# Kernel optimization log

Measured on AMD Instinct MI355X. Metric: run time of the kernel, lower is better.

Reference implementation:

```python
import jax, jax.numpy as jnp
import numpy as np

B, L, DIM, DFF = 4, 2048, 1024, 4096
EPS = 1e-5

def setup_inputs() -> dict:
    key = jax.random.key(0)
    ks = jax.random.split(key, 10)
    s = 0.02
    return {
        "x": jax.random.normal(ks[0], (B, L, DIM), dtype=jnp.float32),
        "ln_g": jnp.ones((DIM,), jnp.float32),
        "ln_b": jnp.zeros((DIM,), jnp.float32),
        "phazor": jax.random.normal(ks[1], (DIM, 2), dtype=jnp.float32),
        "phazor_init": jax.random.normal(ks[2], (DIM, 2), dtype=jnp.float32),
        "w1": jax.random.normal(ks[3], (DIM, DFF), dtype=jnp.float32) * s,
        "b1": jnp.zeros((DFF,), jnp.float32),
        "w2": jax.random.normal(ks[4], (DFF, DIM), dtype=jnp.float32) * s,
        "b2": jnp.zeros((DIM,), jnp.float32),
        "last_conv_re": jax.random.normal(ks[5], (B, DIM), dtype=jnp.float32),
        "last_conv_im": jax.random.normal(ks[6], (B, DIM), dtype=jnp.float32),
    }

def layer_norm(x, g, b):
    mu = jnp.mean(x, axis=-1, keepdims=True)
    var = jnp.var(x, axis=-1, keepdims=True)
    return (x - mu) * jax.lax.rsqrt(var + EPS) * g + b

def spiral_conv(x, phazor, phazor_init, last_re, last_im):
    # x: [B, L, D] float32
    Lx = x.shape[1]
    p = jax.lax.complex(phazor[:, 0], phazor[:, 1])          # [D]
    p_init = jax.lax.complex(phazor_init[:, 0], phazor_init[:, 1])
    pa = jnp.abs(p)
    p = p / pa * jnp.exp(-pa)                                 # normalized decay phazor
    t = jnp.arange(Lx)
    prog = p[None, :] ** t[:, None]                           # [L, D] p^t
    filt = prog * p_init[None, :]                             # [L, D]
    ffilt = jnp.fft.fft(filt, n=2 * Lx, axis=0)               # [2L, D]
    xf = jnp.fft.fft(x.astype(jnp.complex64), n=2 * Lx, axis=1)  # [B, 2L, D]
    conv = jnp.fft.ifft(ffilt[None] * xf, axis=1)[:, :Lx]     # [B, L, D]
    last = jax.lax.complex(last_re, last_im)                  # [B, D] (detached state)
    conv_with_past = conv + last[:, None, :] * prog[None] * p[None, None, :]
    return conv_with_past.real

def reference(x, ln_g, ln_b, phazor, phazor_init, w1, b1, w2, b2, last_conv_re, last_conv_im):
    x_ = x
    h = layer_norm(x, ln_g, ln_b)
    h = spiral_conv(h, phazor, phazor_init, last_conv_re, last_conv_im)
    x = h + x_
    x_ = x
    h = layer_norm(x, ln_g, ln_b)  # same LayerNorm params reused, as in the source
    h = jax.nn.silu(h @ w1 + b1) @ w2 + b2  # FFN, dropout=0 (eval)
    return h + x_

if __name__ == "__main__":
    out = reference(**setup_inputs())
    print(out.shape, out.dtype)
```

## Files before the change

### kernel.cpp

```cpp
#include <hip/hip_runtime.h>
#include <stdint.h>
#include <stddef.h>

#define DIMC 1024
#define LSEQ 2048
#define BSZ  4
#define DFFC 4096
#define NTOK (BSZ*LSEQ)
#define NCHUNK 32
#define CHUNK 64

typedef __bf16 bf16x8 __attribute__((ext_vector_type(8)));
typedef float  f32x4  __attribute__((ext_vector_type(4)));

__device__ __forceinline__ unsigned short f2bf(float f) {
  unsigned int u = __float_as_uint(f);
  u += 0x7fffu + ((u >> 16) & 1u);
  return (unsigned short)(u >> 16);
}

__device__ __forceinline__ void async16(const void* g, void* l) {
  __builtin_amdgcn_global_load_lds(
      (const __attribute__((address_space(1))) unsigned int*)(uintptr_t)g,
      (__attribute__((address_space(3))) unsigned int*)(uintptr_t)l,
      16, 0, 0);
}

__global__ __launch_bounds__(256) void ln_stats(const float* __restrict__ x,
                                                float* __restrict__ mu,
                                                float* __restrict__ rstd) {
  const int token = blockIdx.x;
  const float4* xp = (const float4*)(x + (size_t)token * DIMC);
  float4 v = xp[threadIdx.x];
  float s  = v.x + v.y + v.z + v.w;
  float s2 = v.x*v.x + v.y*v.y + v.z*v.z + v.w*v.w;
  #pragma unroll
  for (int o = 32; o; o >>= 1) { s += __shfl_down(s, o); s2 += __shfl_down(s2, o); }
  __shared__ float sh[8];
  const int lane = threadIdx.x & 63, w = threadIdx.x >> 6;
  if (lane == 0) { sh[w] = s; sh[4 + w] = s2; }
  __syncthreads();
  if (threadIdx.x == 0) {
    float ts  = sh[0] + sh[1] + sh[2] + sh[3];
    float ts2 = sh[4] + sh[5] + sh[6] + sh[7];
    float m = ts * (1.f / DIMC);
    float var = ts2 * (1.f / DIMC) - m * m;
    mu[token] = m;
    rstd[token] = rsqrtf(var + 1e-5f);
  }
}

__global__ __launch_bounds__(256) void ln_apply_bf16(const float* __restrict__ x,
                                                     const float* __restrict__ mu,
                                                     const float* __restrict__ rstd,
                                                     const float* __restrict__ g,
                                                     const float* __restrict__ bb,
                                                     unsigned short* __restrict__ out) {
  const size_t i = (size_t)blockIdx.x * 256 + threadIdx.x;
  float4 v = ((const float4*)x)[i];
  const int token = (int)(i >> 8);
  const int d4 = (int)(i & 255);
  float4 gv = ((const float4*)g)[d4];
  float4 bv = ((const float4*)bb)[d4];
  const float m = mu[token], r = rstd[token];
  ushort4 o;
  o.x = f2bf((v.x - m) * r * gv.x + bv.x);
  o.y = f2bf((v.y - m) * r * gv.y + bv.y);
  o.z = f2bf((v.z - m) * r * gv.z + bv.z);
  o.w = f2bf((v.w - m) * r * gv.w + bv.w);
  ((ushort4*)out)[i] = o;
}

__global__ __launch_bounds__(256) void transpose_bf16(const float* __restrict__ w,
                                                      unsigned short* __restrict__ wt,
                                                      int K, int N) {
  __shared__ float tile[32][33];
  const int n0 = blockIdx.x * 32, k0 = blockIdx.y * 32;
  const int tx = threadIdx.x, ty = threadIdx.y;
  #pragma unroll
  for (int i = 0; i < 32; i += 8)
    tile[ty + i][tx] = w[(size_t)(k0 + ty + i) * N + n0 + tx];
  __syncthreads();
  #pragma unroll
  for (int i = 0; i < 32; i += 8)
    wt[(size_t)(n0 + ty + i) * K + k0 + tx] = f2bf(tile[tx][ty + i]);
}

__device__ __forceinline__ void get_p(const float* __restrict__ phazor, int d,
                                      float& p_re, float& p_im) {
  float pre = phazor[2 * d], pim = phazor[2 * d + 1];
  float a = sqrtf(pre * pre + pim * pim);
  float sc = expf(-a) / a;
  p_re = pre * sc;
  p_im = pim * sc;
}

__global__ __launch_bounds__(256) void scan_phase1(const float* __restrict__ x,
                                                   const float* __restrict__ mu,
                                                   const float* __restrict__ rstd,
                                                   const float* __restrict__ g,
                                                   const float* __restrict__ bb,
                                                   const float* __restrict__ phazor,
                                                   float* __restrict__ Sre,
                                                   float* __restrict__ Sim) {
  const int d = blockIdx.x * 256 + threadIdx.x;
  const int c = blockIdx.y;
  const int b = blockIdx.z;
  float p_re, p_im; get_p(phazor, d, p_re, p_im);
  const float gd = g[d], bd = bb[d];
  const int t0 = c * CHUNK;
  const float* xp  = x + ((size_t)(b * LSEQ + t0)) * DIMC + d;
  const float* mup = mu + b * LSEQ + t0;
  const float* rp  = rstd + b * LSEQ + t0;
  float r_re = 0.f, r_im = 0.f;
  #pragma unroll 4
  for (int s = 0; s < CHUNK; ++s) {
    float hv = (xp[(size_t)s * DIMC] - mup[s]) * rp[s] * gd + bd;
    float nr = p_re * r_re - p_im * r_im + hv;
    float ni = p_re * r_im + p_im * r_re;
    r_re = nr; r_im = ni;
  }
  const int bd_i = b * DIMC + d;
  Sre[c * (BSZ * DIMC) + bd_i] = r_re;
  Sim[c * (BSZ * DIMC) + bd_i] = r_im;
}

__global__ __launch_bounds__(256) void scan_phase2(const float* __restrict__ phazor,
                                                   const float* __restrict__ Sre,
                                                   const float* __restrict__ Sim,
                                                   float* __restrict__ Cre,
                                                   float* __restrict__ Cim) {
  const int bd = blockIdx.x * 256 + threadIdx.x;
  const int d = bd & (DIMC - 1);
  float p_re, p_im; get_p(phazor, d, p_re, p_im);
  float br = p_re, bi = p_im;
  #pragma unroll
  for (int i = 0; i < 6; ++i) { float t = br * br - bi * bi; bi = 2.f * br * bi; br = t; }
  float R_re = 0.f, R_im = 0.f;
  for (int c = 0; c < NCHUNK; ++c) {
    Cre[c * (BSZ * DIMC) + bd] = R_re;
    Cim[c * (BSZ * DIMC) + bd] = R_im;
    float sre = Sre[c * (BSZ * DIMC) + bd], sim = Sim[c * (BSZ * DIMC) + bd];
    float nr = br * R_re - bi * R_im + sre;
    float ni = br * R_im + bi * R_re + sim;
    R_re = nr; R_im = ni;
  }
}

__global__ __launch_bounds__(256) void scan_phase3(const float* __restrict__ x,
                                                   const float* __restrict__ mu,
                                                   const float* __restrict__ rstd,
                                                   const float* __restrict__ g,
                                                   const float* __restrict__ bb,
                                                   const float* __restrict__ phazor,
                                                   const float* __restrict__ phazor_init,
                                                   const float* __restrict__ last_re,
                                                   const float* __restrict__ last_im,
                                                   const float* __restrict__ Cre,
                                                   const float* __restrict__ Cim,
                                                   float* __restrict__ x2) {
  const int d = blockIdx.x * 256 + threadIdx.x;
  const int c = blockIdx.y;
  const int b = blockIdx.z;
  float p_re, p_im; get_p(phazor, d, p_re, p_im);
  const float pi_re = phazor_init[2 * d], pi_im = phazor_init[2 * d + 1];
  const float gd = g[d], bd_ = bb[d];
  const int bd_i = b * DIMC + d;
  float r_re = Cre[c * (BSZ * DIMC) + bd_i];
  float r_im = Cim[c * (BSZ * DIMC) + bd_i];
  float br = p_re, bi = p_im;
  #pragma unroll
  for (int i = 0; i < 6; ++i) { float t = br * br - bi * bi; bi = 2.f * br * bi; br = t; }
  float er = 1.f, ei = 0.f;
  int e = c;
  while (e) {
    if (e & 1) { float t = er * br - ei * bi; ei = er * bi + ei * br; er = t; }
    float t2 = br * br - bi * bi; bi = 2.f * br * bi; br = t2;
    e >>= 1;
  }
  const float lre = last_re[bd_i], lim = last_im[bd_i];
  float q_re = lre * er - lim * ei;
  float q_im = lre * ei + lim * er;
  const int t0 = c * CHUNK;
  const float* xp  = x + ((size_t)(b * LSEQ + t0)) * DIMC + d;
  const float* mup = mu + b * LSEQ + t0;
  const float* rp  = rstd + b * LSEQ + t0;
  float* op = x2 + ((size_t)(b * LSEQ + t0)) * DIMC + d;
  #pragma unroll 4
  for (int s = 0; s < CHUNK; ++s) {
    float xv = xp[(size_t)s * DIMC];
    float hv = (xv - mup[s]) * rp[s] * gd + bd_;
    float nr = p_re * r_re - p_im * r_im + hv;
    float ni = p_re * r_im + p_im * r_re;
    r_re = nr; r_im = ni;
    float nq = p_re * q_re - p_im * q_im;
    q_im = p_re * q_im + p_im * q_re;
    q_re = nq;
    op[(size_t)s * DIMC] = pi_re * r_re - pi_im * r_im + q_re + xv;
  }
}

template <int EPI>
__global__ __launch_bounds__(256) void gemm_bt(const unsigned short* __restrict__ A,
                                               const unsigned short* __restrict__ Bt,
                                               const float* __restrict__ bias,
                                               const float* __restrict__ resid,
                                               void* __restrict__ outp,
                                               int M, int N, int K) {
  __shared__ __align__(16) unsigned short As[128 * 64];
  __shared__ __align__(16) unsigned short Bs[128 * 64];
  const int tid = threadIdx.x;
  const int lane = tid & 63;
  const int bid = blockIdx.x;
  const int ntn = N >> 7;
  const int tm = (bid / ntn) << 7;
  const int tn = (bid % ntn) << 7;
  const int wave = tid >> 6;
  const int wm = (wave & 1) << 6;
  const int wn = (wave >> 1) << 6;

  f32x4 acc[4][4];
  #pragma unroll
  for (int i = 0; i < 4; ++i)
    #pragma unroll
    for (int j = 0; j < 4; ++j) acc[i][j] = (f32x4){0.f, 0.f, 0.f, 0.f};

  const int o0 = tid * 16;
  for (int k0 = 0; k0 < K; k0 += 64) {
    #pragma unroll
    for (int c = 0; c < 4; ++c) {
      const int o = o0 + c * 4096;
      const int r = o >> 7;
      const int ce = (o & 127) >> 1;
      async16(A  + (size_t)(tm + r) * K + (k0 + ce), (char*)As + o);
      async16(Bt + (size_t)(tn + r) * K + (k0 + ce), (char*)Bs + o);
    }
    __syncthreads();
    #pragma unroll
    for (int kk = 0; kk < 2; ++kk) {
      bf16x8 av[4], bv[4];
      #pragma unroll
      for (int i = 0; i < 4; ++i)
        av[i] = *reinterpret_cast<const bf16x8*>(
            As + ((wm + i * 16 + (lane & 15)) << 6) + kk * 32 + ((lane >> 4) << 3));
      #pragma unroll
      for (int i = 0; i < 4; ++i)
        bv[i] = *reinterpret_cast<const bf16x8*>(
            Bs + ((wn + i * 16 + (lane & 15)) << 6) + kk * 32 + ((lane >> 4) << 3));
      #pragma unroll
      for (int mi = 0; mi < 4; ++mi)
        #pragma unroll
        for (int ni = 0; ni < 4; ++ni)
          acc[mi][ni] = __builtin_amdgcn_mfma_f32_16x16x32_bf16(av[mi], bv[ni], acc[mi][ni], 0, 0, 0);
    }
    __syncthreads();
  }

  const int rgrp = (lane >> 4) << 2;
  #pragma unroll
  for (int ni = 0; ni < 4; ++ni) {
    const int n = tn + wn + ni * 16 + (lane & 15);
    const float bv = bias[n];
    #pragma unroll
    for (int mi = 0; mi < 4; ++mi) {
      const int rb = tm + wm + mi * 16 + rgrp;
      #pragma unroll
      for (int j = 0; j < 4; ++j) {
        float v = acc[mi][ni][j] + bv;
        if constexpr (EPI == 0) {
          v = v / (1.f + __expf(-v));
          ((unsigned short*)outp)[(size_t)(rb + j) * N + n] = f2bf(v);
        } else {
          v += resid[(size_t)(rb + j) * N + n];
          ((float*)outp)[(size_t)(rb + j) * N + n] = v;
        }
      }
    }
  }
}

extern "C" void kernel_launch(void* const* d_in, const int* in_sizes, int n_in,
                              void* d_out, int out_size, void* d_ws, size_t ws_size,
                              hipStream_t stream) {
  const float* x           = (const float*)d_in[0];
  const float* ln_g        = (const float*)d_in[1];
  const float* ln_b        = (const float*)d_in[2];
  const float* phazor      = (const float*)d_in[3];
  const float* phazor_init = (const float*)d_in[4];
  const float* w1          = (const float*)d_in[5];
  const float* b1          = (const float*)d_in[6];
  const float* w2          = (const float*)d_in[7];
  const float* b2          = (const float*)d_in[8];
  const float* last_re     = (const float*)d_in[9];
  const float* last_im     = (const float*)d_in[10];
  float* out = (float*)d_out;
  char* ws = (char*)d_ws;
  const size_t MB = 1ull << 20;

  float* x2  = (float*)(ws);
  float* mu1 = (float*)(ws + 32 * MB);
  float* rs1 = (float*)(ws + 32 * MB + 64 * 1024);
  float* mu2 = (float*)(ws + 32 * MB + 128 * 1024);
  float* rs2 = (float*)(ws + 32 * MB + 192 * 1024);
  float* Sre = (float*)(ws + 32 * MB + 256 * 1024);
  float* Sim = (float*)(ws + 32 * MB + 768 * 1024);
  float* Cre = (float*)(ws + 32 * MB + 1280 * 1024);
  float* Cim = (float*)(ws + 32 * MB + 1792 * 1024);
  unsigned short* h2  = (unsigned short*)(ws + 35 * MB);
  unsigned short* hid = (unsigned short*)(ws + 51 * MB);
  unsigned short* w1t = (unsigned short*)(ws + 115 * MB);
  unsigned short* w2t = (unsigned short*)(ws + 123 * MB);

  transpose_bf16<<<dim3(DFFC / 32, DIMC / 32), dim3(32, 8), 0, stream>>>(w1, w1t, DIMC, DFFC);
  transpose_bf16<<<dim3(DIMC / 32, DFFC / 32), dim3(32, 8), 0, stream>>>(w2, w2t, DFFC, DIMC);

  ln_stats<<<NTOK, 256, 0, stream>>>(x, mu1, rs1);
  scan_phase1<<<dim3(DIMC / 256, NCHUNK, BSZ), 256, 0, stream>>>(x, mu1, rs1, ln_g, ln_b, phazor, Sre, Sim);
  scan_phase2<<<(BSZ * DIMC) / 256, 256, 0, stream>>>(phazor, Sre, Sim, Cre, Cim);
  scan_phase3<<<dim3(DIMC / 256, NCHUNK, BSZ), 256, 0, stream>>>(x, mu1, rs1, ln_g, ln_b, phazor,
                                                                 phazor_init, last_re, last_im,
                                                                 Cre, Cim, x2);
  ln_stats<<<NTOK, 256, 0, stream>>>(x2, mu2, rs2);
  ln_apply_bf16<<<NTOK, 256, 0, stream>>>(x2, mu2, rs2, ln_g, ln_b, h2);

  gemm_bt<0><<<(NTOK / 128) * (DFFC / 128), 256, 0, stream>>>(h2, w1t, b1, nullptr, hid, NTOK, DFFC, DIMC);
  gemm_bt<1><<<(NTOK / 128) * (DIMC / 128), 256, 0, stream>>>(hid, w2t, b2, x2, out, NTOK, DIMC, DFFC);
}
```

Measured before the change: 378.9 us.

## Replace FFN GEMMs with 8-wave double-buffered pipelined 256-row tile kernel

```diff
diff --git a/kernel.cpp b/kernel.cpp
--- a/kernel.cpp
+++ b/kernel.cpp
@@ -25,6 +25,16 @@
       (__attribute__((address_space(3))) unsigned int*)(uintptr_t)l,
       16, 0, 0);
 }
+
+__device__ __forceinline__ void bar() {
+  asm volatile("" ::: "memory");
+  __builtin_amdgcn_s_barrier();
+  asm volatile("" ::: "memory");
+}
+#define LGKM0 do { asm volatile("s_waitcnt lgkmcnt(0)" ::: "memory"); \
+                   __builtin_amdgcn_sched_barrier(0); } while (0)
+#define VMCNT(n) asm volatile("s_waitcnt vmcnt(" #n ")" ::: "memory")
+#define MFMA_BF16 __builtin_amdgcn_mfma_f32_16x16x32_bf16
 
 __global__ __launch_bounds__(256) void ln_stats(const float* __restrict__ x,
                                                 float* __restrict__ mu,
@@ -200,70 +210,232 @@
   }
 }
 
-template <int EPI>
-__global__ __launch_bounds__(256) void gemm_bt(const unsigned short* __restrict__ A,
-                                               const unsigned short* __restrict__ Bt,
-                                               const float* __restrict__ bias,
-                                               const float* __restrict__ resid,
-                                               void* __restrict__ outp,
-                                               int M, int N, int K) {
-  __shared__ __align__(16) unsigned short As[128 * 64];
-  __shared__ __align__(16) unsigned short Bs[128 * 64];
-  const int tid = threadIdx.x;
+template<int BN, int EPI>
+__global__ __launch_bounds__(512, 2) void gemm8(const unsigned short* __restrict__ A,
+                                                const unsigned short* __restrict__ Bt,
+                                                const float* __restrict__ bias,
+                                                const float* __restrict__ resid,
+                                                void* __restrict__ outp,
+                                                int M, int N, int K) {
+  constexpr int AUS = 256 * 32;
+  constexpr int BUS = BN * 32;
+  constexpr int BUFUS = 2 * AUS + 2 * BUS;
+  constexpr int NI = BN / 64;
+  __shared__ __align__(16) unsigned short lds[2 * BUFUS];
+
+  const int tid  = threadIdx.x;
   const int lane = tid & 63;
-  const int bid = blockIdx.x;
-  const int ntn = N >> 7;
-  const int tm = (bid / ntn) << 7;
-  const int tn = (bid % ntn) << 7;
   const int wave = tid >> 6;
-  const int wm = (wave & 1) << 6;
-  const int wn = (wave >> 1) << 6;
-
-  f32x4 acc[4][4];
-  #pragma unroll
-  for (int i = 0; i < 4; ++i)
+  const int wm = (wave & 1) * 128;
+  const int wn = (wave >> 1) * (BN / 4);
+  const int r15 = lane & 15;
+  const int cus = ((lane >> 4) ^ ((r15 >> 1) & 3)) * 8;
+
+  int bid = blockIdx.x;
+  const int cpx = gridDim.x >> 3;
+  bid = (bid & 7) * cpx + (bid >> 3);
+  const int ntn = N / BN;
+  const int tm = (bid / ntn) * 256;
+  const int tn = (bid % ntn) * BN;
+  const int NT = K >> 6;
+
+  f32x4 acc[8][NI];
+  #pragma unroll
+  for (int i = 0; i < 8; ++i)
     #pragma unroll
-    for (int j = 0; j < 4; ++j) acc[i][j] = (f32x4){0.f, 0.f, 0.f, 0.f};
-
-  const int o0 = tid * 16;
-  for (int k0 = 0; k0 < K; k0 += 64) {
+    for (int j = 0; j < NI; ++j) acc[i][j] = (f32x4){0.f, 0.f, 0.f, 0.f};
+
+  auto stageA = [&](int buf, int kk, int k0) {
+    unsigned short* blk = lds + buf * BUFUS + kk * AUS;
+    const unsigned short* g = A + (size_t)tm * K + k0 + kk * 32;
     #pragma unroll
-    for (int c = 0; c < 4; ++c) {
-      const int o = o0 + c * 4096;
-      const int r = o >> 7;
-      const int ce = (o & 127) >> 1;
-      async16(A  + (size_t)(tm + r) * K + (k0 + ce), (char*)As + o);
-      async16(Bt + (size_t)(tn + r) * K + (k0 + ce), (char*)Bs + o);
+    for (int r = 0; r < 2; ++r) {
+      const int s = r * 512 + tid;
+      const int row = s >> 2;
+      const int cg = (s & 3) ^ ((s >> 3) & 3);
+      async16(g + (size_t)row * K + cg * 8, blk + (size_t)s * 8);
     }
-    __syncthreads();
+  };
+  auto stageB = [&](int buf, int kk, int k0) {
+    unsigned short* blk = lds + buf * BUFUS + 2 * AUS + kk * BUS;
+    const unsigned short* g = Bt + (size_t)tn * K + k0 + kk * 32;
     #pragma unroll
-    for (int kk = 0; kk < 2; ++kk) {
-      bf16x8 av[4], bv[4];
-      #pragma unroll
-      for (int i = 0; i < 4; ++i)
-        av[i] = *reinterpret_cast<const bf16x8*>(
-            As + ((wm + i * 16 + (lane & 15)) << 6) + kk * 32 + ((lane >> 4) << 3));
-      #pragma unroll
-      for (int i = 0; i < 4; ++i)
-        bv[i] = *reinterpret_cast<const bf16x8*>(
-            Bs + ((wn + i * 16 + (lane & 15)) << 6) + kk * 32 + ((lane >> 4) << 3));
-      #pragma unroll
-      for (int mi = 0; mi < 4; ++mi)
-        #pragma unroll
-        for (int ni = 0; ni < 4; ++ni)
-          acc[mi][ni] = __builtin_amdgcn_mfma_f32_16x16x32_bf16(av[mi], bv[ni], acc[mi][ni], 0, 0, 0);
+    for (int r = 0; r < BN / 128; ++r) {
+      const int s = r * 512 + tid;
+      const int row = s >> 2;
+      const int cg = (s & 3) ^ ((s >> 3) & 3);
+      async16(g + (size_t)row * K + cg * 8, blk + (size_t)s * 8);
     }
-    __syncthreads();
-  }
-
-  const int rgrp = (lane >> 4) << 2;
-  #pragma unroll
-  for (int ni = 0; ni < 4; ++ni) {
-    const int n = tn + wn + ni * 16 + (lane & 15);
+  };
+  auto rdA = [&](int buf, int kk, int mi) -> bf16x8 {
+    return *(const bf16x8*)(lds + buf * BUFUS + kk * AUS + (wm + mi * 16 + r15) * 32 + cus);
+  };
+  auto rdB = [&](int buf, int kk, int ni) -> bf16x8 {
+    return *(const bf16x8*)(lds + buf * BUFUS + 2 * AUS + kk * BUS + (wn + ni * 16 + r15) * 32 + cus);
+  };
+
+  bf16x8 af[8], bq0, bq1;
+
+  stageA(0, 0, 0); stageB(0, 0, 0); stageA(0, 1, 0); stageB(0, 1, 0);
+  if constexpr (BN == 256) VMCNT(4); else VMCNT(3);
+  bar();
+
+  for (int t = 0; t < NT - 1; ++t) {
+    const int buf = t & 1, nb = buf ^ 1, kn = (t + 1) << 6;
+    if constexpr (BN == 256) {
+      #pragma unroll
+      for (int mi = 0; mi < 8; ++mi) af[mi] = rdA(buf, 0, mi);
+      bq0 = rdB(buf, 0, 0); bq1 = rdB(buf, 0, 1);
+      stageA(nb, 0, kn);
+      bar(); LGKM0;
+      __builtin_amdgcn_s_setprio(1);
+      #pragma unroll
+      for (int mi = 0; mi < 8; ++mi) {
+        acc[mi][0] = MFMA_BF16(af[mi], bq0, acc[mi][0], 0, 0, 0);
+        acc[mi][1] = MFMA_BF16(af[mi], bq1, acc[mi][1], 0, 0, 0);
+      }
+      __builtin_amdgcn_s_setprio(0);
+      bar();
+      bq0 = rdB(buf, 0, 2); bq1 = rdB(buf, 0, 3);
+      stageB(nb, 0, kn);
+      bar(); LGKM0;
+      __builtin_amdgcn_s_setprio(1);
+      #pragma unroll
+      for (int mi = 0; mi < 8; ++mi) {
+        acc[mi][2] = MFMA_BF16(af[mi], bq0, acc[mi][2], 0, 0, 0);
+        acc[mi][3] = MFMA_BF16(af[mi], bq1, acc[mi][3], 0, 0, 0);
+      }
+      __builtin_amdgcn_s_setprio(0);
+      VMCNT(4);
+      bar();
+      #pragma unroll
+      for (int mi = 0; mi < 8; ++mi) af[mi] = rdA(buf, 1, mi);
+      bq0 = rdB(buf, 1, 0); bq1 = rdB(buf, 1, 1);
+      stageA(nb, 1, kn);
+      bar(); LGKM0;
+      __builtin_amdgcn_s_setprio(1);
+      #pragma unroll
+      for (int mi = 0; mi < 8; ++mi) {
+        acc[mi][0] = MFMA_BF16(af[mi], bq0, acc[mi][0], 0, 0, 0);
+        acc[mi][1] = MFMA_BF16(af[mi], bq1, acc[mi][1], 0, 0, 0);
+      }
+      __builtin_amdgcn_s_setprio(0);
+      bar();
+      bq0 = rdB(buf, 1, 2); bq1 = rdB(buf, 1, 3);
+      stageB(nb, 1, kn);
+      bar(); LGKM0;
+      __builtin_amdgcn_s_setprio(1);
+      #pragma unroll
+      for (int mi = 0; mi < 8; ++mi) {
+        acc[mi][2] = MFMA_BF16(af[mi], bq0, acc[mi][2], 0, 0, 0);
+        acc[mi][3] = MFMA_BF16(af[mi], bq1, acc[mi][3], 0, 0, 0);
+      }
+      __builtin_amdgcn_s_setprio(0);
+      VMCNT(4);
+      bar();
+    } else {
+      #pragma unroll
+      for (int mi = 0; mi < 8; ++mi) af[mi] = rdA(buf, 0, mi);
+      bq0 = rdB(buf, 0, 0); bq1 = rdB(buf, 0, 1);
+      stageA(nb, 0, kn); stageB(nb, 0, kn);
+      bar(); LGKM0;
+      __builtin_amdgcn_s_setprio(1);
+      #pragma unroll
+      for (int mi = 0; mi < 8; ++mi) {
+        acc[mi][0] = MFMA_BF16(af[mi], bq0, acc[mi][0], 0, 0, 0);
+        acc[mi][1] = MFMA_BF16(af[mi], bq1, acc[mi][1], 0, 0, 0);
+      }
+      __builtin_amdgcn_s_setprio(0);
+      VMCNT(3);
+      bar();
+      #pragma unroll
+      for (int mi = 0; mi < 8; ++mi) af[mi] = rdA(buf, 1, mi);
+      bq0 = rdB(buf, 1, 0); bq1 = rdB(buf, 1, 1);
+      stageA(nb, 1, kn); stageB(nb, 1, kn);
+      bar(); LGKM0;
+      __builtin_amdgcn_s_setprio(1);
+      #pragma unroll
+      for (int mi = 0; mi < 8; ++mi) {
+        acc[mi][0] = MFMA_BF16(af[mi], bq0, acc[mi][0], 0, 0, 0);
+        acc[mi][1] = MFMA_BF16(af[mi], bq1, acc[mi][1], 0, 0, 0);
+      }
+      __builtin_amdgcn_s_setprio(0);
+      VMCNT(3);
+      bar();
+    }
+  }
+
+  {
+    const int buf = (NT - 1) & 1;
+    if constexpr (BN == 256) {
+      #pragma unroll
+      for (int mi = 0; mi < 8; ++mi) af[mi] = rdA(buf, 0, mi);
+      bq0 = rdB(buf, 0, 0); bq1 = rdB(buf, 0, 1);
+      bar(); LGKM0;
+      #pragma unroll
+      for (int mi = 0; mi < 8; ++mi) {
+        acc[mi][0] = MFMA_BF16(af[mi], bq0, acc[mi][0], 0, 0, 0);
+        acc[mi][1] = MFMA_BF16(af[mi], bq1, acc[mi][1], 0, 0, 0);
+      }
+      bar();
+      bq0 = rdB(buf, 0, 2); bq1 = rdB(buf, 0, 3);
+      bar(); LGKM0;
+      #pragma unroll
+      for (int mi = 0; mi < 8; ++mi) {
+        acc[mi][2] = MFMA_BF16(af[mi], bq0, acc[mi][2], 0, 0, 0);
+        acc[mi][3] = MFMA_BF16(af[mi], bq1, acc[mi][3], 0, 0, 0);
+      }
+      VMCNT(0);
+      bar();
+      #pragma unroll
+      for (int mi = 0; mi < 8; ++mi) af[mi] = rdA(buf, 1, mi);
+      bq0 = rdB(buf, 1, 0); bq1 = rdB(buf, 1, 1);
+      bar(); LGKM0;
+      #pragma unroll
+      for (int mi = 0; mi < 8; ++mi) {
+        acc[mi][0] = MFMA_BF16(af[mi], bq0, acc[mi][0], 0, 0, 0);
+        acc[mi][1] = MFMA_BF16(af[mi], bq1, acc[mi][1], 0, 0, 0);
+      }
+      bar();
+      bq0 = rdB(buf, 1, 2); bq1 = rdB(buf, 1, 3);
+      LGKM0;
+      #pragma unroll
+      for (int mi = 0; mi < 8; ++mi) {
+        acc[mi][2] = MFMA_BF16(af[mi], bq0, acc[mi][2], 0, 0, 0);
+        acc[mi][3] = MFMA_BF16(af[mi], bq1, acc[mi][3], 0, 0, 0);
+      }
+    } else {
+      #pragma unroll
+      for (int mi = 0; mi < 8; ++mi) af[mi] = rdA(buf, 0, mi);
+      bq0 = rdB(buf, 0, 0); bq1 = rdB(buf, 0, 1);
+      bar(); LGKM0;
+      #pragma unroll
+      for (int mi = 0; mi < 8; ++mi) {
+        acc[mi][0] = MFMA_BF16(af[mi], bq0, acc[mi][0], 0, 0, 0);
+        acc[mi][1] = MFMA_BF16(af[mi], bq1, acc[mi][1], 0, 0, 0);
+      }
+      VMCNT(0);
+      bar();
+      #pragma unroll
+      for (int mi = 0; mi < 8; ++mi) af[mi] = rdA(buf, 1, mi);
+      bq0 = rdB(buf, 1, 0); bq1 = rdB(buf, 1, 1);
+      LGKM0;
+      #pragma unroll
+      for (int mi = 0; mi < 8; ++mi) {
+        acc[mi][0] = MFMA_BF16(af[mi], bq0, acc[mi][0], 0, 0, 0);
+        acc[mi][1] = MFMA_BF16(af[mi], bq1, acc[mi][1], 0, 0, 0);
+      }
+    }
+  }
+
+  const int rg = (lane >> 4) * 4;
+  #pragma unroll
+  for (int ni = 0; ni < NI; ++ni) {
+    const int n = tn + wn + ni * 16 + r15;
     const float bv = bias[n];
     #pragma unroll
-    for (int mi = 0; mi < 4; ++mi) {
-      const int rb = tm + wm + mi * 16 + rgrp;
+    for (int mi = 0; mi < 8; ++mi) {
+      const int rb = tm + wm + mi * 16 + rg;
       #pragma unroll
       for (int j = 0; j < 4; ++j) {
         float v = acc[mi][ni][j] + bv;
@@ -323,6 +495,8 @@
   ln_stats<<<NTOK, 256, 0, stream>>>(x2, mu2, rs2);
   ln_apply_bf16<<<NTOK, 256, 0, stream>>>(x2, mu2, rs2, ln_g, ln_b, h2);
 
-  gemm_bt<0><<<(NTOK / 128) * (DFFC / 128), 256, 0, stream>>>(h2, w1t, b1, nullptr, hid, NTOK, DFFC, DIMC);
-  gemm_bt<1><<<(NTOK / 128) * (DIMC / 128), 256, 0, stream>>>(hid, w2t, b2, x2, out, NTOK, DIMC, DFFC);
-}
+  gemm8<256, 0><<<(NTOK / 256) * (DFFC / 256), 512, 0, stream>>>(h2, w1t, b1, nullptr, hid,
+                                                                 NTOK, DFFC, DIMC);
+  gemm8<128, 1><<<(NTOK / 256) * (DIMC / 128), 512, 0, stream>>>(hid, w2t, b2, x2, out,
+                                                                 NTOK, DIMC, DFFC);
+}
```

Measured after the change: 329.3 us. 13.1% less time.
